# Kernel tuning notes

Hardware: AMD Instinct MI355X
Metric: run time of the kernel (lower is better)

Reference implementation:

```python
import jax, jax.numpy as jnp
import numpy as np

ALPHA = 1.0
BETA = 1.0


def setup_inputs() -> dict:
    key = jax.random.key(0)
    k1, k2, k3, k4 = jax.random.split(key, 4)
    B_, S, D_in, D_out, R = 4, 64, 8192, 8192, 16
    x = jax.random.normal(k1, (B_, S, D_in), dtype=jnp.float32)
    original_weight = jax.random.normal(k2, (D_out, D_in), dtype=jnp.float32) * 0.02
    A = jax.random.normal(k3, (D_out, R), dtype=jnp.float32) * 0.02
    Bm = jax.random.normal(k4, (R, D_in), dtype=jnp.float32) * 0.02
    return {"x": x, "original_weight": original_weight, "A": A, "B": Bm}


def reference(x, original_weight, A, B):
    # delta_weight = alpha * (A @ B)  -> [D_out, D_in]
    delta_weight = ALPHA * jnp.matmul(A, B)
    # F.linear(x, W + beta*delta) = x @ (W + beta*delta)^T
    W = original_weight + BETA * delta_weight
    return jnp.einsum("bsd,od->bso", x, W)
```

## Files before the change

kernel.cpp:

```cpp
#include <hip/hip_runtime.h>
#include <stdint.h>


#define DM 256
#define DK 8192
#define DN 8192
#define RLORA 16

#define TN 64
#define BK 64
#define KSPLIT 4
#define KCHUNK (DK / KSPLIT)
#define NITER (KCHUNK / BK)

typedef short bf16x8 __attribute__((ext_vector_type(8)));
typedef float f32x4v __attribute__((ext_vector_type(4)));

__device__ __forceinline__ unsigned short f2bf(float f) {
  unsigned u = __builtin_bit_cast(unsigned, f);
  u += 0x7FFFu + ((u >> 16) & 1u);
  return (unsigned short)(u >> 16);
}

__device__ __forceinline__ bf16x8 pack8(float4 a, float4 b) {
  bf16x8 r;
  r[0] = (short)f2bf(a.x); r[1] = (short)f2bf(a.y);
  r[2] = (short)f2bf(a.z); r[3] = (short)f2bf(a.w);
  r[4] = (short)f2bf(b.x); r[5] = (short)f2bf(b.y);
  r[6] = (short)f2bf(b.z); r[7] = (short)f2bf(b.w);
  return r;
}

__global__ __launch_bounds__(256) void prep_x(
    const float* __restrict__ x, const float* __restrict__ Bm,
    unsigned short* __restrict__ xb, float* __restrict__ y32) {
  const int ks = blockIdx.x;
  const int m0 = blockIdx.y * 4;
  const int t = threadIdx.x;
  const int k = ks * 1024 + t * 4;
  const int K64 = k >> 6, s = (k >> 5) & 1, oct = (k >> 3) & 3;
  const int e = k & 7;
  float4 xv[4];
#pragma unroll
  for (int i = 0; i < 4; ++i) {
    const int m = m0 + i;
    const int g = m >> 4, r = m & 15;
    xv[i] = *(const float4*)(x + (size_t)m * DK + k);
    ushort4 h;
    h.x = f2bf(xv[i].x); h.y = f2bf(xv[i].y);
    h.z = f2bf(xv[i].z); h.w = f2bf(xv[i].w);
    const size_t chunk = (size_t)(K64 * 32 + s * 16 + g) * 64 + oct * 16 + r;
    *(ushort4*)(xb + chunk * 8 + e) = h;
  }
  float acc[4][RLORA];
#pragma unroll
  for (int r = 0; r < RLORA; ++r) {
    float4 b = *(const float4*)(Bm + (size_t)r * DK + k);
#pragma unroll
    for (int i = 0; i < 4; ++i)
      acc[i][r] = xv[i].x * b.x + xv[i].y * b.y + xv[i].z * b.z + xv[i].w * b.w;
  }
#pragma unroll
  for (int off = 32; off >= 1; off >>= 1)
#pragma unroll
    for (int i = 0; i < 4; ++i)
#pragma unroll
      for (int r = 0; r < RLORA; ++r)
        acc[i][r] += __shfl_xor(acc[i][r], off, 64);
  __shared__ float red[4][4][RLORA];
  const int lane = t & 63, wv = t >> 6;
  if (lane == 0) {
#pragma unroll
    for (int i = 0; i < 4; ++i)
#pragma unroll
      for (int r = 0; r < RLORA; ++r) red[wv][i][r] = acc[i][r];
  }
  __syncthreads();
  if (t < 64) {
    int i = t >> 4, r = t & 15;
    float sum = red[0][i][r] + red[1][i][r] + red[2][i][r] + red[3][i][r];
    atomicAdd(y32 + (m0 + i) * RLORA + r, sum);
  }
}

__global__ __launch_bounds__(512, 4) void lora_gemm(
    const unsigned short* __restrict__ xb,
    const float* __restrict__ W,
    const float* __restrict__ y32,
    const float* __restrict__ Aw,
    float* __restrict__ out,
    float* __restrict__ part) {
  __shared__ unsigned short wsm[2][4096];

  const int tid = threadIdx.x;
  const int lane = tid & 63, w = tid >> 6;
  const int qr = lane & 15, quad = lane >> 4;

  const int bid = blockIdx.x;
  const int xcd = bid & 7;
  const int kz = xcd >> 1;
  const int nblk = (bid >> 3) + ((xcd & 1) << 6);
  const int n0 = nblk * TN;
  const int kb = kz * KCHUNK;

  const int Fs = w >> 2, Fsub = w & 3;
  const float* wsrc = W + (size_t)(n0 + Fsub * 16 + qr) * DK + kb +
                      Fs * 32 + quad * 8;
  const unsigned wdst = (unsigned)tid * 16;

  const bf16x8* ap = (const bf16x8*)xb + ((size_t)(kz * 32) * 32) * 64 + lane;

  f32x4v acc[2][4];
#pragma unroll
  for (int a = 0; a < 2; ++a)
#pragma unroll
    for (int b = 0; b < 4; ++b) acc[a][b] = (f32x4v){0.f, 0.f, 0.f, 0.f};

  float4 g0 = *(const float4*)(wsrc);
  float4 g1 = *(const float4*)(wsrc + 4);
  *(bf16x8*)((char*)wsm[0] + wdst) = pack8(g0, g1);
  __syncthreads();

  for (int it = 0; it < NITER; ++it) {
    bf16x8 av[2][2];
#pragma unroll
    for (int s = 0; s < 2; ++s)
#pragma unroll
      for (int mt = 0; mt < 2; ++mt)
        av[mt][s] = ap[(size_t)(s * 16 + w * 2 + mt) * 64];
    ap += (size_t)32 * 64;
    const bool havW = (it + 1 < NITER);
    if (havW) {
      const float* p = wsrc + (size_t)(it + 1) * BK;
      g0 = *(const float4*)(p);
      g1 = *(const float4*)(p + 4);
    }
    const char* wcur = (const char*)wsm[it & 1];
#pragma unroll
    for (int s = 0; s < 2; ++s) {
      bf16x8 b[4];
#pragma unroll
      for (int sub = 0; sub < 4; ++sub)
        b[sub] = *(const bf16x8*)(wcur + (((s * 4 + sub) * 64 + lane) * 16));
#pragma unroll
      for (int mt = 0; mt < 2; ++mt)
#pragma unroll
        for (int sub = 0; sub < 4; ++sub)
          acc[mt][sub] = __builtin_amdgcn_mfma_f32_16x16x32_bf16(
              av[mt][s], b[sub], acc[mt][sub], 0, 0, 0);
    }
    if (havW) *(bf16x8*)((char*)wsm[(it + 1) & 1] + wdst) = pack8(g0, g1);
    __syncthreads();
  }

  if (kz == 0) {
    const float4 z = {0.f, 0.f, 0.f, 0.f};
    bf16x8 b[4];
#pragma unroll
    for (int sub = 0; sub < 4; ++sub) {
      const float* ap2 = Aw + (size_t)(n0 + sub * 16 + qr) * RLORA + quad * 8;
      float4 p0 = (quad < 2) ? *(const float4*)(ap2) : z;
      float4 p1 = (quad < 2) ? *(const float4*)(ap2 + 4) : z;
      b[sub] = pack8(p0, p1);
    }
#pragma unroll
    for (int mt = 0; mt < 2; ++mt) {
      const float* yp = y32 + (size_t)(w * 32 + mt * 16 + qr) * RLORA + quad * 8;
      float4 q0 = (quad < 2) ? *(const float4*)(yp) : z;
      float4 q1 = (quad < 2) ? *(const float4*)(yp + 4) : z;
      bf16x8 avt = pack8(q0, q1);
#pragma unroll
      for (int sub = 0; sub < 4; ++sub)
        acc[mt][sub] = __builtin_amdgcn_mfma_f32_16x16x32_bf16(
            avt, b[sub], acc[mt][sub], 0, 0, 0);
    }
  }

  if (part) {
    float* pb = part + (size_t)kz * DM * DN;
#pragma unroll
    for (int mt = 0; mt < 2; ++mt)
#pragma unroll
      for (int sub = 0; sub < 4; ++sub) {
        float* p = pb + (size_t)(w * 32 + mt * 16 + quad * 4) * DN +
                   n0 + sub * 16 + qr;
#pragma unroll
        for (int rg = 0; rg < 4; ++rg) p[(size_t)rg * DN] = acc[mt][sub][rg];
      }
  } else {
    float* ob = out;
#pragma unroll
    for (int mt = 0; mt < 2; ++mt)
#pragma unroll
      for (int sub = 0; sub < 4; ++sub) {
        float* p = ob + (size_t)(w * 32 + mt * 16 + quad * 4) * DN +
                   n0 + sub * 16 + qr;
#pragma unroll
        for (int rg = 0; rg < 4; ++rg)
          atomicAdd(p + (size_t)rg * DN, acc[mt][sub][rg]);
      }
  }
}

__global__ __launch_bounds__(256) void reduce_k(
    const float* __restrict__ part, float* __restrict__ out) {
  size_t i = ((size_t)blockIdx.x * 256 + threadIdx.x) * 4;
  float4 s = *(const float4*)(part + i);
#pragma unroll
  for (int kzi = 1; kzi < KSPLIT; ++kzi) {
    float4 v = *(const float4*)(part + (size_t)kzi * DM * DN + i);
    s.x += v.x; s.y += v.y; s.z += v.z; s.w += v.w;
  }
  *(float4*)(out + i) = s;
}

extern "C" void kernel_launch(void* const* d_in, const int* in_sizes, int n_in,
                              void* d_out, int out_size, void* d_ws, size_t ws_size,
                              hipStream_t stream) {
  const float* x  = (const float*)d_in[0];
  const float* W  = (const float*)d_in[1];
  const float* A  = (const float*)d_in[2];
  const float* Bm = (const float*)d_in[3];
  float* out = (float*)d_out;

  unsigned short* xb = (unsigned short*)d_ws;
  float* y32 = (float*)((char*)d_ws + (4u << 20));
  size_t base_bytes = (4u << 20) + 16384;
  size_t part_bytes = (size_t)KSPLIT * DM * DN * 4;
  bool use_part = ws_size >= base_bytes + part_bytes;
  float* part = use_part ? (float*)((char*)d_ws + base_bytes) : nullptr;

  if (!use_part)
    hipMemsetAsync(d_out, 0, (size_t)out_size * sizeof(float), stream);
  hipMemsetAsync(y32, 0, (size_t)DM * RLORA * sizeof(float), stream);
  prep_x<<<dim3(8, 64), 256, 0, stream>>>(x, Bm, xb, y32);
  lora_gemm<<<512, 512, 0, stream>>>(xb, W, y32, A, out, part);
  if (use_part) reduce_k<<<2048, 256, 0, stream>>>(part, out);
}
```

Measured before the change: 425.5 us.

## Double K-tile to 128 and prefetch W two iterations ahead in registers

Raises the K-step from 64 to 128, so each thread now loads and packs two W fragments per iteration into a doubled shared buffer. That halves the number of barrier syncs. W global loads are issued two iterations ahead using a two-slot register ring, and x fragments are loaded in two halves so loads overlap the MFMA work. The cost is more registers per thread, with occupancy risk under launch_bounds(512,4), and twice the LDS per block.

```diff
diff --git a/kernel.cpp b/kernel.cpp
--- a/kernel.cpp
+++ b/kernel.cpp
@@ -8,7 +8,7 @@
 #define RLORA 16
 
 #define TN 64
-#define BK 64
+#define BK 128
 #define KSPLIT 4
 #define KCHUNK (DK / KSPLIT)
 #define NITER (KCHUNK / BK)
@@ -90,7 +90,7 @@
     const float* __restrict__ Aw,
     float* __restrict__ out,
     float* __restrict__ part) {
-  __shared__ unsigned short wsm[2][4096];
+  __shared__ unsigned short wsm[2][8192];
 
   const int tid = threadIdx.x;
   const int lane = tid & 63, w = tid >> 6;
@@ -103,10 +103,13 @@
   const int n0 = nblk * TN;
   const int kb = kz * KCHUNK;
 
-  const int Fs = w >> 2, Fsub = w & 3;
-  const float* wsrc = W + (size_t)(n0 + Fsub * 16 + qr) * DK + kb +
-                      Fs * 32 + quad * 8;
-  const unsigned wdst = (unsigned)tid * 16;
+  const int f0 = w * 2, f1 = f0 + 1;
+  const float* wsrc0 = W + (size_t)(n0 + (f0 & 3) * 16 + qr) * DK + kb +
+                       (f0 >> 2) * 32 + quad * 8;
+  const float* wsrc1 = W + (size_t)(n0 + (f1 & 3) * 16 + qr) * DK + kb +
+                       (f1 >> 2) * 32 + quad * 8;
+  const unsigned wdst0 = (unsigned)(f0 * 64 + lane) * 16;
+  const unsigned wdst1 = wdst0 + 1024;
 
   const bf16x8* ap = (const bf16x8*)xb + ((size_t)(kz * 32) * 32) * 64 + lane;
 
@@ -116,26 +119,29 @@
 #pragma unroll
     for (int b = 0; b < 4; ++b) acc[a][b] = (f32x4v){0.f, 0.f, 0.f, 0.f};
 
-  float4 g0 = *(const float4*)(wsrc);
-  float4 g1 = *(const float4*)(wsrc + 4);
-  *(bf16x8*)((char*)wsm[0] + wdst) = pack8(g0, g1);
+  float4 g[2][4];
+  g[0][0] = *(const float4*)(wsrc0);
+  g[0][1] = *(const float4*)(wsrc0 + 4);
+  g[0][2] = *(const float4*)(wsrc1);
+  g[0][3] = *(const float4*)(wsrc1 + 4);
+  g[1][0] = *(const float4*)(wsrc0 + BK);
+  g[1][1] = *(const float4*)(wsrc0 + BK + 4);
+  g[1][2] = *(const float4*)(wsrc1 + BK);
+  g[1][3] = *(const float4*)(wsrc1 + BK + 4);
+  *(bf16x8*)((char*)wsm[0] + wdst0) = pack8(g[0][0], g[0][1]);
+  *(bf16x8*)((char*)wsm[0] + wdst1) = pack8(g[0][2], g[0][3]);
   __syncthreads();
 
+#pragma unroll 2
   for (int it = 0; it < NITER; ++it) {
+    const char* wcur = (const char*)wsm[it & 1];
     bf16x8 av[2][2];
 #pragma unroll
-    for (int s = 0; s < 2; ++s)
-#pragma unroll
-      for (int mt = 0; mt < 2; ++mt)
-        av[mt][s] = ap[(size_t)(s * 16 + w * 2 + mt) * 64];
-    ap += (size_t)32 * 64;
-    const bool havW = (it + 1 < NITER);
-    if (havW) {
-      const float* p = wsrc + (size_t)(it + 1) * BK;
-      g0 = *(const float4*)(p);
-      g1 = *(const float4*)(p + 4);
-    }
-    const char* wcur = (const char*)wsm[it & 1];
+    for (int si = 0; si < 2; ++si)
+#pragma unroll
+      for (int mt = 0; mt < 2; ++mt)
+        av[si][mt] =
+            ap[(size_t)((it * 2) * 32 + si * 16 + w * 2 + mt) * 64];
 #pragma unroll
     for (int s = 0; s < 2; ++s) {
       bf16x8 b[4];
@@ -147,9 +153,40 @@
 #pragma unroll
         for (int sub = 0; sub < 4; ++sub)
           acc[mt][sub] = __builtin_amdgcn_mfma_f32_16x16x32_bf16(
-              av[mt][s], b[sub], acc[mt][sub], 0, 0, 0);
-    }
-    if (havW) *(bf16x8*)((char*)wsm[(it + 1) & 1] + wdst) = pack8(g0, g1);
+              av[s][mt], b[sub], acc[mt][sub], 0, 0, 0);
+    }
+#pragma unroll
+    for (int si = 0; si < 2; ++si)
+#pragma unroll
+      for (int mt = 0; mt < 2; ++mt)
+        av[si][mt] =
+            ap[(size_t)((it * 2 + 1) * 32 + si * 16 + w * 2 + mt) * 64];
+    if (it + 2 < NITER) {
+      const float* p0 = wsrc0 + (size_t)(it + 2) * BK;
+      const float* p1 = wsrc1 + (size_t)(it + 2) * BK;
+      g[it & 1][0] = *(const float4*)(p0);
+      g[it & 1][1] = *(const float4*)(p0 + 4);
+      g[it & 1][2] = *(const float4*)(p1);
+      g[it & 1][3] = *(const float4*)(p1 + 4);
+    }
+#pragma unroll
+    for (int s = 2; s < 4; ++s) {
+      bf16x8 b[4];
+#pragma unroll
+      for (int sub = 0; sub < 4; ++sub)
+        b[sub] = *(const bf16x8*)(wcur + (((s * 4 + sub) * 64 + lane) * 16));
+#pragma unroll
+      for (int mt = 0; mt < 2; ++mt)
+#pragma unroll
+        for (int sub = 0; sub < 4; ++sub)
+          acc[mt][sub] = __builtin_amdgcn_mfma_f32_16x16x32_bf16(
+              av[s - 2][mt], b[sub], acc[mt][sub], 0, 0, 0);
+    }
+    if (it + 1 < NITER) {
+      char* wnxt = (char*)wsm[(it + 1) & 1];
+      *(bf16x8*)(wnxt + wdst0) = pack8(g[(it + 1) & 1][0], g[(it + 1) & 1][1]);
+      *(bf16x8*)(wnxt + wdst1) = pack8(g[(it + 1) & 1][2], g[(it + 1) & 1][3]);
+    }
     __syncthreads();
   }
 
```

New measurement: 422.0 us. About the same (-0.8%).
